# Kernel tuning notes

Measured on AMD Instinct MI355X. Metric: run time of the kernel, lower is better.

## Reference

```python
import jax, jax.numpy as jnp
import numpy as np

N, E, IN, K, F, D = 50000, 800000, 256, 4, 64, 2


def setup_inputs() -> dict:
    key = jax.random.key(0)
    ks = jax.random.split(key, 10)
    # CSR rowptr: 0 .. E, nondecreasing, endpoints pinned
    inner = jnp.sort(jax.random.randint(ks[0], (N - 1,), 0, E + 1))
    rowptr = jnp.concatenate([jnp.zeros(1, jnp.int64), inner.astype(jnp.int64), jnp.full(1, E, jnp.int64)])
    colind = jax.random.randint(ks[1], (E,), 0, N).astype(jnp.int64)
    # CSC mirrors (used only by the fused kernel's backward; inert in forward math)
    inner_c = jnp.sort(jax.random.randint(ks[2], (N - 1,), 0, E + 1))
    colptr = jnp.concatenate([jnp.zeros(1, jnp.int64), inner_c.astype(jnp.int64), jnp.full(1, E, jnp.int64)])
    rowind = jax.random.randint(ks[3], (E,), 0, N).astype(jnp.int64)
    permute = jnp.arange(E, dtype=jnp.int64)
    feat = jax.random.normal(ks[4], (N, IN), dtype=jnp.float32)
    pseudo = jax.random.uniform(ks[5], (E, D), dtype=jnp.float32)
    # params: fc weight [K*F, IN] (xavier-normal style scale), mu ~ N(0, 0.1), inv_sigma = 1, bias = 0
    gain = float(np.sqrt(2.0))
    std = gain * float(np.sqrt(2.0 / (IN + K * F)))
    W_fc = jax.random.normal(ks[6], (K * F, IN), dtype=jnp.float32) * std
    mu = jax.random.normal(ks[7], (K, D), dtype=jnp.float32) * 0.1
    inv_sigma = jnp.ones((K, D), dtype=jnp.float32)
    bias = jnp.zeros((F,), dtype=jnp.float32)
    return {"rowptr": rowptr, "colind": colind, "colptr": colptr, "rowind": rowind,
            "permute": permute, "feat": feat, "pseudo": pseudo,
            "W_fc": W_fc, "mu": mu, "inv_sigma": inv_sigma, "bias": bias}


def reference(rowptr, colind, colptr, rowind, permute, feat, pseudo, W_fc, mu, inv_sigma, bias):
    n = feat.shape[0]
    e = colind.shape[0]
    k, d = mu.shape
    f = W_fc.shape[0] // k
    # dense projection: [N, K, F]
    node_feat = (feat @ W_fc.T).reshape(n, k, f)
    # per-edge Gaussian mixture weights: [E, K]
    diff = pseudo[:, None, :] - mu[None, :, :]              # [E, K, D]
    gaussian = jnp.exp(jnp.sum(-0.5 * diff * diff * (inv_sigma[None, :, :] ** 2), axis=-1))
    # multi-head SpMM: gather source feats, weight per kernel, sum kernels (sum commutes
    # with the segment reduction, so fold the head-sum into the edge message): [E, F]
    msg = jnp.einsum('ek,ekf->ef', gaussian, node_feat[colind])
    # destination node of each CSR edge
    dst = jnp.searchsorted(rowptr, jnp.arange(e), side='right') - 1
    rst = jax.ops.segment_sum(msg, dst, num_segments=n)      # [N, F]
    return rst + bias
```

## Files before the change

### kernel.cpp

```cpp
#include <hip/hip_runtime.h>


typedef _Float16 f16;
typedef __attribute__((ext_vector_type(4))) _Float16 f16x4;
typedef __attribute__((ext_vector_type(8))) _Float16 f16x8;
typedef __attribute__((ext_vector_type(4))) float f32x4;

__device__ inline f16x4 cvt4h(float4 v) {
    f16x4 h;
    h.x = (f16)v.x; h.y = (f16)v.y; h.z = (f16)v.z; h.w = (f16)v.w;
    return h;
}

__device__ inline int dot4_i8(int a, int b) {
#if __has_builtin(__builtin_amdgcn_sdot4)
    return __builtin_amdgcn_sdot4(a, b, 0, false);
#else
    return (int)(char)(a)       * (int)(char)(b)
         + (int)(char)(a >> 8)  * (int)(char)(b >> 8)
         + (int)(char)(a >> 16) * (int)(char)(b >> 16)
         + (int)(char)(a >> 24) * (int)(char)(b >> 24);
#endif
}

__global__ __launch_bounds__(256) void convert_W(
    const float* __restrict__ W, f16* __restrict__ Wp)
{
    const int gid = blockIdx.x * 256 + threadIdx.x;
    const int jp = gid >> 6, k4 = gid & 63;
    const int wrow = ((jp & 3) << 6) | (jp >> 2);
    reinterpret_cast<f16x4*>(Wp)[jp * 64 + k4] =
        cvt4h(reinterpret_cast<const float4*>(W)[wrow * 64 + k4]);
}

#define ASTRIDE 264
#define AS_BYTES (64 * ASTRIDE * 2)

__global__ __launch_bounds__(256) void gemm_fused(
    const float* __restrict__ feat,
    const f16* __restrict__ Wp,
    char* __restrict__ nfq,
    float* __restrict__ sc,
    int M)
{
    __shared__ char smem[AS_BYTES + 256 * 32 * 2];
    f16* As = (f16*)smem;
    f16* Bs = (f16*)(smem + AS_BYTES);
    char* qt = smem + AS_BYTES;
    const int t    = threadIdx.x;
    const int lane = t & 63;
    const int wave = t >> 6;
    const int bm   = blockIdx.x * 64;
    const int l16  = lane & 15;
    const int quad = lane >> 4;
    const int wn   = wave * 64;

    size_t bsrc[4];
#pragma unroll
    for (int j = 0; j < 4; ++j)
        bsrc[j] = (size_t)(wave * 64 + j * 16 + (lane >> 2)) * 256 + (lane & 3) * 8;

    typedef __attribute__((address_space(3))) void lds_t;
    typedef const __attribute__((address_space(1))) void gm_t;

#pragma unroll
    for (int j = 0; j < 4; ++j)
        __builtin_amdgcn_global_load_lds((gm_t*)(Wp + bsrc[j]),
            (lds_t*)(Bs + (wave * 4 + j) * 512), 16, 0, 0);

#pragma unroll
    for (int it = 0; it < 8; ++it) {
        const int flat = it * 2048 + t * 8;
        const int row  = flat >> 8;
        const int koff = flat & 255;
        const float* src = feat + (size_t)min(bm + row, M - 1) * 256 + koff;
        const float4 a0 = *reinterpret_cast<const float4*>(src);
        const float4 a1 = *reinterpret_cast<const float4*>(src + 4);
        *reinterpret_cast<f16x4*>(&As[row * ASTRIDE + koff])     = cvt4h(a0);
        *reinterpret_cast<f16x4*>(&As[row * ASTRIDE + koff + 4]) = cvt4h(a1);
    }

    f32x4 acc[4][4];
#pragma unroll
    for (int mi = 0; mi < 4; ++mi)
#pragma unroll
        for (int ni = 0; ni < 4; ++ni)
            acc[mi][ni] = (f32x4){0.f, 0.f, 0.f, 0.f};

    for (int ki = 0; ki < 8; ++ki) {
        __syncthreads();

        f16x8 af[4], bfr[4];
#pragma unroll
        for (int mi = 0; mi < 4; ++mi)
            af[mi] = *reinterpret_cast<const f16x8*>(
                &As[(mi * 16 + l16) * ASTRIDE + ki * 32 + quad * 8]);
#pragma unroll
        for (int ni = 0; ni < 4; ++ni)
            bfr[ni] = *reinterpret_cast<const f16x8*>(
                &Bs[(wn + ni * 16 + l16) * 32 + quad * 8]);

        __syncthreads();
        if (ki < 7) {
            const int k0 = (ki + 1) * 32;
#pragma unroll
            for (int j = 0; j < 4; ++j)
                __builtin_amdgcn_global_load_lds((gm_t*)(Wp + bsrc[j] + k0),
                    (lds_t*)(Bs + (wave * 4 + j) * 512), 16, 0, 0);
        }
#pragma unroll
        for (int mi = 0; mi < 4; ++mi)
#pragma unroll
            for (int ni = 0; ni < 4; ++ni)
                acc[mi][ni] = __builtin_amdgcn_mfma_f32_16x16x32_f16(
                    af[mi], bfr[ni], acc[mi][ni], 0, 0, 0);
    }

#pragma unroll
    for (int mi = 0; mi < 4; ++mi) {
#pragma unroll
        for (int r = 0; r < 4; ++r) {
            float am = 0.f;
#pragma unroll
            for (int ni = 0; ni < 4; ++ni)
                am = fmaxf(am, fabsf(acc[mi][ni][r]));
            am = fmaxf(am, __shfl_xor(am, 1));
            am = fmaxf(am, __shfl_xor(am, 2));
            am = fmaxf(am, __shfl_xor(am, 4));
            am = fmaxf(am, __shfl_xor(am, 8));
            const float sinv = am > 0.f ? 127.f / am : 0.f;
            const int rl = mi * 16 + quad * 4 + r;
#pragma unroll
            for (int ni = 0; ni < 4; ++ni)
                qt[rl * 256 + wn + ni * 16 + l16] =
                    (char)(int)__builtin_rintf(acc[mi][ni][r] * sinv);
            if (l16 == 0) {
                const int row = bm + rl;
                if (row < M) sc[row * 4 + wave] = am * (1.f / 16129.f);
            }
        }
    }
    __syncthreads();

    {
        const int rl  = t >> 2;
        const int co  = (t & 3) * 64;
        const int row = bm + rl;
        if (row < M) {
            const int4* s4 = reinterpret_cast<const int4*>(qt + rl * 256 + co);
            int4* d4 = reinterpret_cast<int4*>(nfq + (size_t)row * 256 + co);
#pragma unroll
            for (int j = 0; j < 4; ++j) d4[j] = s4[j];
        }
    }
}

__global__ __launch_bounds__(256) void edge_aggregate(
    const int* __restrict__ rowptr,
    const int* __restrict__ colind,
    const float* __restrict__ pseudo,
    const char* __restrict__ nfq,
    const float* __restrict__ sc,
    const float* __restrict__ mu,
    const float* __restrict__ inv_sigma,
    const float* __restrict__ bias,
    float* __restrict__ out,
    int N)
{
    const int lane = threadIdx.x & 63;
    const int wid  = blockIdx.x * 4 + (threadIdx.x >> 6);
    const int na   = wid * 2;
    if (na >= N) return;
    const int nb   = na + 1;
    const bool hb  = nb < N;

    const int fo   = lane & 15;
    const int eg   = lane >> 4;
    const int qoff = fo << 4;
    const int goff = fo >> 2;

    float mxk[4], myk[4], cxk[4], cyk[4];
#pragma unroll
    for (int k = 0; k < 4; ++k) {
        mxk[k] = mu[2 * k];
        myk[k] = mu[2 * k + 1];
        const float a = inv_sigma[2 * k], b = inv_sigma[2 * k + 1];
        const float c = -0.5f * 1.4426950408889634f;
        cxk[k] = c * a * a;
        cyk[k] = c * b * b;
    }

    auto gpack = [&](int ec, int e0, int e1) -> int {
        const int exm = ec + fo;
        const bool gv = exm < e1;
        const int safe = (e1 > e0) ? (e1 - 1) : 0;
        const int ex  = gv ? exm : safe;
        const float2 p = *reinterpret_cast<const float2*>(pseudo + 2 * (size_t)ex);
        int gp = 0;
#pragma unroll
        for (int k = 0; k < 4; ++k) {
            const float dx = p.x - mxk[k], dy = p.y - myk[k];
            const float g = exp2f(fmaf(dy * dy, cyk[k], dx * dx * cxk[k]));
            gp |= ((int)(g * 127.f + 0.5f)) << (8 * k);
        }
        return gv ? gp : 0;
    };

    const int ea0 = rowptr[na];
    const int ea1 = rowptr[na + 1];
    const int eb0 = ea1;
    const int eb1 = hb ? rowptr[nb + 1] : ea1;

    const int safea = (ea1 > ea0) ? (ea1 - 1) : 0;
    int cfo_a = colind[min(ea0 + fo, safea)];
    int cfo_b = 0, gpk_b = 0;
    if (hb) {
        const int safeb = (eb1 > eb0) ? (eb1 - 1) : 0;
        cfo_b = colind[min(eb0 + fo, safeb)];
        gpk_b = gpack(eb0, eb0, eb1);
    }
    int gpk_a = gpack(ea0, ea0, ea1);

    float a0 = 0.f, a1 = 0.f, a2 = 0.f, a3 = 0.f;
    {
        int gpk = gpk_a, cfo = cfo_a;
        for (int ec = ea0; ec < ea1; ec += 16) {
            int4  q[4];
            float s[4];
            int   gq[4];
#pragma unroll
            for (int gi = 0; gi < 4; ++gi) {
                const int c = __shfl(cfo, gi * 4 + eg);
                q[gi]  = *reinterpret_cast<const int4*>(
                             nfq + ((size_t)c << 8) + qoff);
                s[gi]  = sc[c * 4 + goff];
                gq[gi] = __shfl(gpk, gi * 4 + eg);
            }
            const int ecn = ec + 16;
            int gpk_n = 0, cfo_n = cfo;
            if (ecn < ea1) {
                cfo_n = colind[min(ecn + fo, ea1 - 1)];
                gpk_n = gpack(ecn, ea0, ea1);
            }
#pragma unroll
            for (int gi = 0; gi < 4; ++gi) {
                a0 = fmaf(s[gi], (float)dot4_i8(q[gi].x, gq[gi]), a0);
                a1 = fmaf(s[gi], (float)dot4_i8(q[gi].y, gq[gi]), a1);
                a2 = fmaf(s[gi], (float)dot4_i8(q[gi].z, gq[gi]), a2);
                a3 = fmaf(s[gi], (float)dot4_i8(q[gi].w, gq[gi]), a3);
            }
            gpk = gpk_n; cfo = cfo_n;
        }
    }
    a0 += __shfl_xor(a0, 16); a0 += __shfl_xor(a0, 32);
    a1 += __shfl_xor(a1, 16); a1 += __shfl_xor(a1, 32);
    a2 += __shfl_xor(a2, 16); a2 += __shfl_xor(a2, 32);
    a3 += __shfl_xor(a3, 16); a3 += __shfl_xor(a3, 32);
    if (lane < 16) {
        const float4 b4 = reinterpret_cast<const float4*>(bias)[fo];
        float4 o;
        o.x = a0 + b4.x; o.y = a1 + b4.y; o.z = a2 + b4.z; o.w = a3 + b4.w;
        reinterpret_cast<float4*>(out + ((size_t)na << 6))[fo] = o;
    }

    if (!hb) return;
    float b0 = 0.f, b1 = 0.f, b2 = 0.f, b3 = 0.f;
    {
        int gpk = gpk_b, cfo = cfo_b;
        for (int ec = eb0; ec < eb1; ec += 16) {
            int4  q[4];
            float s[4];
            int   gq[4];
#pragma unroll
            for (int gi = 0; gi < 4; ++gi) {
                const int c = __shfl(cfo, gi * 4 + eg);
                q[gi]  = *reinterpret_cast<const int4*>(
                             nfq + ((size_t)c << 8) + qoff);
                s[gi]  = sc[c * 4 + goff];
                gq[gi] = __shfl(gpk, gi * 4 + eg);
            }
            const int ecn = ec + 16;
            int gpk_n = 0, cfo_n = cfo;
            if (ecn < eb1) {
                cfo_n = colind[min(ecn + fo, eb1 - 1)];
                gpk_n = gpack(ecn, eb0, eb1);
            }
#pragma unroll
            for (int gi = 0; gi < 4; ++gi) {
                b0 = fmaf(s[gi], (float)dot4_i8(q[gi].x, gq[gi]), b0);
                b1 = fmaf(s[gi], (float)dot4_i8(q[gi].y, gq[gi]), b1);
                b2 = fmaf(s[gi], (float)dot4_i8(q[gi].z, gq[gi]), b2);
                b3 = fmaf(s[gi], (float)dot4_i8(q[gi].w, gq[gi]), b3);
            }
            gpk = gpk_n; cfo = cfo_n;
        }
    }
    b0 += __shfl_xor(b0, 16); b0 += __shfl_xor(b0, 32);
    b1 += __shfl_xor(b1, 16); b1 += __shfl_xor(b1, 32);
    b2 += __shfl_xor(b2, 16); b2 += __shfl_xor(b2, 32);
    b3 += __shfl_xor(b3, 16); b3 += __shfl_xor(b3, 32);
    if (lane < 16) {
        const float4 b4 = reinterpret_cast<const float4*>(bias)[fo];
        float4 o;
        o.x = b0 + b4.x; o.y = b1 + b4.y; o.z = b2 + b4.z; o.w = b3 + b4.w;
        reinterpret_cast<float4*>(out + ((size_t)nb << 6))[fo] = o;
    }
}

extern "C" void kernel_launch(void* const* d_in, const int* in_sizes, int n_in,
                              void* d_out, int out_size, void* d_ws, size_t ws_size,
                              hipStream_t stream)
{
    const int*   rowptr    = (const int*)d_in[0];
    const int*   colind    = (const int*)d_in[1];
    const float* feat      = (const float*)d_in[5];
    const float* pseudo    = (const float*)d_in[6];
    const float* W_fc      = (const float*)d_in[7];
    const float* mu        = (const float*)d_in[8];
    const float* inv_sigma = (const float*)d_in[9];
    const float* bias      = (const float*)d_in[10];
    float* out = (float*)d_out;

    const int N = in_sizes[0] - 1;
    char*  nfq = (char*)d_ws;
    float* sc  = (float*)(nfq + (size_t)N * 256);
    f16*   Wp  = (f16*)d_out;

    hipLaunchKernelGGL(convert_W, dim3(64), dim3(256), 0, stream, W_fc, Wp);

    hipLaunchKernelGGL(gemm_fused, dim3((N + 63) / 64), dim3(256), 0, stream,
                       feat, Wp, nfq, sc, N);

    hipLaunchKernelGGL(edge_aggregate, dim3((N + 7) / 8), dim3(256), 0, stream,
                       rowptr, colind, pseudo, nfq, sc, mu, inv_sigma, bias, out, N);
}
```

Before: 165.8 us.

## Double-buffer B tile, XOR-swizzle LDS layouts, spread Gaussian kernels across lanes

The GEMM now double-buffers the W tile in LDS, issuing the next global_load_lds before the MFMAs and waiting on vmcnt instead of two __syncthreads per k-step. A and B LDS tiles switch from padded strides to XOR-swizzled layouts, with the W pre-conversion writing swizzled columns to match. This is meant to hide load latency and avoid bank conflicts. In the SpMM kernel, each 16-lane group computes one of the four Gaussian kernels and combines them with shuffles, cutting per-lane exp work at the cost of two cross-lane shuffles.

```diff
diff --git a/kernel.cpp b/kernel.cpp
--- a/kernel.cpp
+++ b/kernel.cpp
@@ -29,12 +29,10 @@
     const int gid = blockIdx.x * 256 + threadIdx.x;
     const int jp = gid >> 6, k4 = gid & 63;
     const int wrow = ((jp & 3) << 6) | (jp >> 2);
-    reinterpret_cast<f16x4*>(Wp)[jp * 64 + k4] =
+    const int k4s = k4 ^ ((jp & 3) << 1);
+    reinterpret_cast<f16x4*>(Wp)[jp * 64 + k4s] =
         cvt4h(reinterpret_cast<const float4*>(W)[wrow * 64 + k4]);
 }
-
-#define ASTRIDE 264
-#define AS_BYTES (64 * ASTRIDE * 2)
 
 __global__ __launch_bounds__(256) void gemm_fused(
     const float* __restrict__ feat,
@@ -43,10 +41,10 @@
     float* __restrict__ sc,
     int M)
 {
-    __shared__ char smem[AS_BYTES + 256 * 32 * 2];
-    f16* As = (f16*)smem;
-    f16* Bs = (f16*)(smem + AS_BYTES);
-    char* qt = smem + AS_BYTES;
+    __shared__ char smem[32768 + 2 * 16384];
+    char* Asb = smem;
+    char* BsB = smem + 32768;
+    char* qt  = BsB;
     const int t    = threadIdx.x;
     const int lane = t & 63;
     const int wave = t >> 6;
@@ -66,7 +64,7 @@
 #pragma unroll
     for (int j = 0; j < 4; ++j)
         __builtin_amdgcn_global_load_lds((gm_t*)(Wp + bsrc[j]),
-            (lds_t*)(Bs + (wave * 4 + j) * 512), 16, 0, 0);
+            (lds_t*)(BsB + (wave * 4 + j) * 1024), 16, 0, 0);
 
 #pragma unroll
     for (int it = 0; it < 8; ++it) {
@@ -76,8 +74,9 @@
         const float* src = feat + (size_t)min(bm + row, M - 1) * 256 + koff;
         const float4 a0 = *reinterpret_cast<const float4*>(src);
         const float4 a1 = *reinterpret_cast<const float4*>(src + 4);
-        *reinterpret_cast<f16x4*>(&As[row * ASTRIDE + koff])     = cvt4h(a0);
-        *reinterpret_cast<f16x4*>(&As[row * ASTRIDE + koff + 4]) = cvt4h(a1);
+        char* dst = Asb + row * 512 + ((koff * 2) ^ ((row & 7) << 4));
+        *reinterpret_cast<f16x4*>(dst)     = cvt4h(a0);
+        *reinterpret_cast<f16x4*>(dst + 8) = cvt4h(a1);
     }
 
     f32x4 acc[4][4];
@@ -87,27 +86,40 @@
         for (int ni = 0; ni < 4; ++ni)
             acc[mi][ni] = (f32x4){0.f, 0.f, 0.f, 0.f};
 
+    __syncthreads();
+
+    const int axor = (l16 & 7) << 4;
+    const int bxor = (l16 & 3) << 4;
+
+#pragma unroll
     for (int ki = 0; ki < 8; ++ki) {
-        __syncthreads();
+        const char* bsb = BsB + ((ki & 1) << 14);
+        if (ki < 7) {
+            const int k0 = (ki + 1) * 32;
+            char* dstb = BsB + (((ki + 1) & 1) << 14);
+#pragma unroll
+            for (int j = 0; j < 4; ++j)
+                __builtin_amdgcn_global_load_lds((gm_t*)(Wp + bsrc[j] + k0),
+                    (lds_t*)(dstb + (wave * 4 + j) * 1024), 16, 0, 0);
+            __builtin_amdgcn_sched_barrier(0);
+            asm volatile("s_waitcnt vmcnt(4)" ::: "memory");
+            __builtin_amdgcn_sched_barrier(0);
+        } else {
+            __builtin_amdgcn_sched_barrier(0);
+            asm volatile("s_waitcnt vmcnt(0)" ::: "memory");
+            __builtin_amdgcn_sched_barrier(0);
+        }
 
         f16x8 af[4], bfr[4];
 #pragma unroll
         for (int mi = 0; mi < 4; ++mi)
             af[mi] = *reinterpret_cast<const f16x8*>(
-                &As[(mi * 16 + l16) * ASTRIDE + ki * 32 + quad * 8]);
+                Asb + (mi * 16 + l16) * 512 + ((ki * 64 + quad * 16) ^ axor));
 #pragma unroll
         for (int ni = 0; ni < 4; ++ni)
             bfr[ni] = *reinterpret_cast<const f16x8*>(
-                &Bs[(wn + ni * 16 + l16) * 32 + quad * 8]);
-
-        __syncthreads();
-        if (ki < 7) {
-            const int k0 = (ki + 1) * 32;
-#pragma unroll
-            for (int j = 0; j < 4; ++j)
-                __builtin_amdgcn_global_load_lds((gm_t*)(Wp + bsrc[j] + k0),
-                    (lds_t*)(Bs + (wave * 4 + j) * 512), 16, 0, 0);
-        }
+                bsb + (wn + ni * 16 + l16) * 64 + ((quad << 4) ^ bxor));
+
 #pragma unroll
         for (int mi = 0; mi < 4; ++mi)
 #pragma unroll
@@ -115,6 +127,8 @@
                 acc[mi][ni] = __builtin_amdgcn_mfma_f32_16x16x32_f16(
                     af[mi], bfr[ni], acc[mi][ni], 0, 0, 0);
     }
+
+    __syncthreads();
 
 #pragma unroll
     for (int mi = 0; mi < 4; ++mi) {
@@ -179,16 +193,12 @@
     const int qoff = fo << 4;
     const int goff = fo >> 2;
 
-    float mxk[4], myk[4], cxk[4], cyk[4];
-#pragma unroll
-    for (int k = 0; k < 4; ++k) {
-        mxk[k] = mu[2 * k];
-        myk[k] = mu[2 * k + 1];
-        const float a = inv_sigma[2 * k], b = inv_sigma[2 * k + 1];
-        const float c = -0.5f * 1.4426950408889634f;
-        cxk[k] = c * a * a;
-        cyk[k] = c * b * b;
-    }
+    const int kk = lane >> 4;
+    const float mx = mu[2 * kk], my = mu[2 * kk + 1];
+    const float sa = inv_sigma[2 * kk], sb = inv_sigma[2 * kk + 1];
+    const float C  = -0.5f * 1.4426950408889634f;
+    const float cx = C * sa * sa, cy = C * sb * sb;
+    const int   sh = kk * 8;
 
     auto gpack = [&](int ec, int e0, int e1) -> int {
         const int exm = ec + fo;
@@ -196,14 +206,12 @@
         const int safe = (e1 > e0) ? (e1 - 1) : 0;
         const int ex  = gv ? exm : safe;
         const float2 p = *reinterpret_cast<const float2*>(pseudo + 2 * (size_t)ex);
-        int gp = 0;
-#pragma unroll
-        for (int k = 0; k < 4; ++k) {
-            const float dx = p.x - mxk[k], dy = p.y - myk[k];
-            const float g = exp2f(fmaf(dy * dy, cyk[k], dx * dx * cxk[k]));
-            gp |= ((int)(g * 127.f + 0.5f)) << (8 * k);
-        }
-        return gv ? gp : 0;
+        const float dx = p.x - mx, dy = p.y - my;
+        const float g = exp2f(fmaf(dy * dy, cy, dx * dx * cx));
+        int b = gv ? (((int)(g * 127.f + 0.5f)) << sh) : 0;
+        b |= __shfl_xor(b, 16);
+        b |= __shfl_xor(b, 32);
+        return b;
     };
 
     const int ea0 = rowptr[na];
```

Measured after the change: 166.0 us. Within noise of the previous version (+0.1%).
